# Kernel tuning notes

Measured on AMD Instinct MI355X. Metric: run time of the kernel, lower is better.

## Reference

```python
import jax, jax.numpy as jnp
import numpy as np

SIGMA = 1.0
MU = 1.0
STRIKE = 3.0
N_STEPS = 256
BATCH = 131072


def setup_inputs() -> dict:
    key = jax.random.key(0)
    ks = jax.random.split(key, 4)

    def lin(k, o, i):
        # equinox Linear-style uniform init in [-1/sqrt(i), 1/sqrt(i)]
        lim = 1.0 / np.sqrt(i)
        return jax.random.uniform(k, (o, i), jnp.float32, -lim, lim)

    return {
        "noise": jax.random.normal(ks[0], (N_STEPS, BATCH), jnp.float32),
        "ts": jnp.linspace(0.0, 1.0, N_STEPS + 1, dtype=jnp.float32),
        "w": jnp.float32(0.9),  # E[max(S1 - K, 0)] Monte-Carlo constant
        "W1": lin(ks[1], 32, 2), "b1": jnp.zeros((32,), jnp.float32),
        "W2": lin(ks[2], 32, 32), "b2": jnp.zeros((32,), jnp.float32),
        "W3": lin(ks[3], 1, 32), "b3": jnp.zeros((1,), jnp.float32),
    }


def reference(noise, ts, w, W1, b1, W2, b2, W3, b3):
    # Holding strategy MLP: in=[t, s] (2) -> 32 -> 32 -> 1, silu/silu/sigmoid
    def holding(t, s):  # s: [B] -> h: [B]
        x = jnp.stack([jnp.broadcast_to(t, s.shape), s], axis=-1)  # [B,2]
        a = jax.nn.silu(x @ W1.T + b1)
        a = jax.nn.silu(a @ W2.T + b2)
        return jax.nn.sigmoid(a @ W3.T + b3)[:, 0]

    def drift(t, y):  # y: [B,2] -> [B,2]
        s = y[:, 0]
        h = holding(t, s)
        return jnp.stack([MU * s, MU * s * h], axis=-1)

    def diffusion(t, y):  # scalar Brownian noise: diffusion vector [B,2]
        s = y[:, 0]
        h = holding(t, s)
        return jnp.stack([SIGMA * s, SIGMA * s * h], axis=-1)

    dts = jnp.diff(ts)                      # [N]
    dWs = noise * jnp.sqrt(dts)[:, None]    # [N,B] Brownian increments

    def step(y, xs):
        t, dt, dW = xs                      # dW: [B]
        f = drift(t, y)
        g = diffusion(t, y)
        # Milstein correction: directional derivative (Dg . g) via jvp
        _, dg = jax.jvp(lambda yy: diffusion(t, yy), (y,), (g,))
        y1 = (y + f * dt + g * dW[:, None]
              + 0.5 * dg * (dW * dW - dt)[:, None])  # Ito Milstein
        return y1, None

    B = noise.shape[1]
    y0 = jnp.broadcast_to(jnp.array([1.0, 0.0], jnp.float32), (B, 2))
    yT, _ = jax.lax.scan(step, y0, (ts[:-1], dts, dWs))

    s1 = yT[:, 0]
    hedging_pnl = yT[:, 1]
    z = jnp.maximum(0.0, s1 - STRIKE)
    return (z - hedging_pnl - w) ** 2  # [B] per-path loss
```

## Files before the change

kernel.cpp:

```cpp
#include <hip/hip_runtime.h>
#include <hip/hip_fp16.h>
#include <math.h>

#define BATCH 131072
#define NSTEPS 256
#define SEGLEN 64
#define NSEG 4
#define LGN 7
#define NPTS 128
#define ZSPAN 12.0f
#define ZLO 6.0f
#define ZSCALE (NPTS / ZSPAN)
#define DZ (ZSPAN / NPTS)
#define MU_C 0.72134752044448170367f
#define SD_C 1.4426950408889634f

using f32x2 = __attribute__((ext_vector_type(2))) float;

__device__ __forceinline__ float fast_exp(float x) {
    return __builtin_amdgcn_exp2f(x * 1.44269504088896340736f);
}
__device__ __forceinline__ float fast_rcp(float x) {
    return __builtin_amdgcn_rcpf(x);
}
__device__ __forceinline__ float sigmoidf_fast(float x) {
    return fast_rcp(1.0f + fast_exp(-x));
}

#define REP32(M) M(0) M(1) M(2) M(3) M(4) M(5) M(6) M(7) \
                 M(8) M(9) M(10) M(11) M(12) M(13) M(14) M(15) \
                 M(16) M(17) M(18) M(19) M(20) M(21) M(22) M(23) \
                 M(24) M(25) M(26) M(27) M(28) M(29) M(30) M(31)

#define REP8(M) M(0) M(1) M(2) M(3) M(4) M(5) M(6) M(7)

#define MLP_BODY(W1r, B1, W2r, B2, W3r, b3v, t, s, sd, H, HACC) \
    { \
        const float __t = (t), __s = (s), __sd = (sd); \
        f32x2 acc2 = {(b3v), 0.0f}; \
        REP32(MLP_L1) \
        REP32(MLP_ROW) \
        H = sigmoidf_fast(acc2.x); \
        HACC = acc2.y; \
    }

#define MLP_L1(j) f32x2 at##j; { \
    const float2 wv = W1r[j]; \
    const float z  = fmaf(wv.x, __t, fmaf(wv.y, __s, B1[j])); \
    const float zd = wv.y * __sd; \
    const float sg = sigmoidf_fast(z); \
    const float da = sg * (1.0f + z * (1.0f - sg)); \
    at##j = (f32x2){z * sg, da * zd}; }

#define MLP_ROW(j) { \
    const float4 q0 = W2r[(j) * 8 + 0]; \
    const float4 q1 = W2r[(j) * 8 + 1]; \
    const float4 q2 = W2r[(j) * 8 + 2]; \
    const float4 q3 = W2r[(j) * 8 + 3]; \
    const float4 q4 = W2r[(j) * 8 + 4]; \
    const float4 q5 = W2r[(j) * 8 + 5]; \
    const float4 q6 = W2r[(j) * 8 + 6]; \
    const float4 q7 = W2r[(j) * 8 + 7]; \
    f32x2 zza = {B2[j], 0.0f}; \
    f32x2 zzb = {0.0f, 0.0f}; \
    zza += (f32x2){q0.x, q0.x} * at0;  zzb += (f32x2){q0.y, q0.y} * at1; \
    zza += (f32x2){q0.z, q0.z} * at2;  zzb += (f32x2){q0.w, q0.w} * at3; \
    zza += (f32x2){q1.x, q1.x} * at4;  zzb += (f32x2){q1.y, q1.y} * at5; \
    zza += (f32x2){q1.z, q1.z} * at6;  zzb += (f32x2){q1.w, q1.w} * at7; \
    zza += (f32x2){q2.x, q2.x} * at8;  zzb += (f32x2){q2.y, q2.y} * at9; \
    zza += (f32x2){q2.z, q2.z} * at10; zzb += (f32x2){q2.w, q2.w} * at11; \
    zza += (f32x2){q3.x, q3.x} * at12; zzb += (f32x2){q3.y, q3.y} * at13; \
    zza += (f32x2){q3.z, q3.z} * at14; zzb += (f32x2){q3.w, q3.w} * at15; \
    zza += (f32x2){q4.x, q4.x} * at16; zzb += (f32x2){q4.y, q4.y} * at17; \
    zza += (f32x2){q4.z, q4.z} * at18; zzb += (f32x2){q4.w, q4.w} * at19; \
    zza += (f32x2){q5.x, q5.x} * at20; zzb += (f32x2){q5.y, q5.y} * at21; \
    zza += (f32x2){q5.z, q5.z} * at22; zzb += (f32x2){q5.w, q5.w} * at23; \
    zza += (f32x2){q6.x, q6.x} * at24; zzb += (f32x2){q6.y, q6.y} * at25; \
    zza += (f32x2){q6.z, q6.z} * at26; zzb += (f32x2){q6.w, q6.w} * at27; \
    zza += (f32x2){q7.x, q7.x} * at28; zzb += (f32x2){q7.y, q7.y} * at29; \
    zza += (f32x2){q7.z, q7.z} * at30; zzb += (f32x2){q7.w, q7.w} * at31; \
    const f32x2 zzt = zza + zzb; \
    const float zv  = zzt.x; \
    const float sg  = sigmoidf_fast(zv); \
    const float da  = sg * (1.0f + zv * (1.0f - sg)); \
    const float w3  = W3r[j]; \
    acc2 += (f32x2){w3, w3} * (f32x2){zv * sg, da * zzt.y}; \
}

__global__ __launch_bounds__(256) void table_eval_kernel(
    const float* __restrict__ ts,
    const float* __restrict__ W1, const float* __restrict__ b1,
    const float* __restrict__ W2, const float* __restrict__ b2,
    const float* __restrict__ W3, const float* __restrict__ b3,
    unsigned int* __restrict__ W)
{
    __shared__ __align__(16) float sW1[64];
    __shared__ float sb1[32];
    __shared__ __align__(16) float sW2[1024];
    __shared__ float sb2[32];
    __shared__ float sW3[32];
    __shared__ float sb3[1];

    const int tid = threadIdx.x;
    for (int i = tid; i < 1024; i += 256) sW2[i] = W2[i];
    if (tid < 64) sW1[tid] = W1[tid];
    if (tid < 32) { sb1[tid] = b1[tid]; sb2[tid] = b2[tid]; sW3[tid] = W3[tid]; }
    if (tid == 0) sb3[0] = b3[0];
    __syncthreads();

    const float2* W1r = (const float2*)sW1;
    const float*  B1  = sb1;
    const float4* W2r = (const float4*)sW2;
    const float*  B2  = sb2;
    const float*  W3r = sW3;
    const float   b3v = sb3[0];

    const int gid = blockIdx.x * 256 + tid;
    const int st = gid >> LGN;
    const int k  = gid & (NPTS - 1);

    const float t  = ts[st];
    const float mu = MU_C * t;
    const float sd = SD_C * __builtin_sqrtf(t) + 1e-4f;
    const float zz = fmaf((float)k, DZ, -ZLO);
    const float s  = __builtin_amdgcn_exp2f(fmaf(zz, sd, mu));

    float h, hacc;
    MLP_BODY(W1r, B1, W2r, B2, W3r, b3v, t, s, 1.0f, h, hacc)

    const float q = h * (1.0f - h) * hacc * s;
    __half2 p = __floats2half2_rn(h, q);
    const unsigned int pv = *(unsigned int*)&p;

    W[2 * gid] = pv;
    if (k > 0)         W[2 * gid - 1] = pv;
    if (k == NPTS - 1) W[2 * gid + 1] = pv;
}

__global__ __launch_bounds__(256) void prod_kernel(
    const float* __restrict__ noise,
    const float* __restrict__ ts,
    float* __restrict__ P)
{
    __shared__ float2 sdt[SEGLEN];
    const int g    = blockIdx.x >> 9;
    const int pblk = blockIdx.x & 511;
    const int tid  = threadIdx.x;
    const int sbase = g * SEGLEN;

    if (tid < SEGLEN) {
        const float t0 = ts[sbase + tid];
        const float dtv = ts[sbase + tid + 1] - t0;
        sdt[tid] = make_float2(dtv, __builtin_sqrtf(dtv));
    }
    __syncthreads();

    const int path = pblk * 256 + tid;
    const float* np_ = noise + (size_t)sbase * BATCH + path;

    float prod = 1.0f;
    #pragma unroll 8
    for (int k = 0; k < SEGLEN; ++k) {
        const float2 d = sdt[k];
        const float dW  = np_[(size_t)k * BATCH] * d.y;
        const float mil = 0.5f * fmaf(dW, dW, -d.x);
        const float A   = d.x + dW + mil;
        prod = fmaf(prod, A, prod);
    }
    P[(size_t)g * BATCH + path] = prod;
}

__global__ __launch_bounds__(256, 4) void seg_kernel(
    const float* __restrict__ noise,
    const float* __restrict__ ts,
    const uint2* __restrict__ T2,
    const float* __restrict__ P,
    float* __restrict__ pnlb,
    float* __restrict__ sT,
    float* __restrict__ out)
{
    __shared__ float4 sdt4[SEGLEN];
    __shared__ float  scr[SEGLEN];
    const int g    = blockIdx.x >> 9;
    const int pblk = blockIdx.x & 511;
    const int tid  = threadIdx.x;
    const int sbase = g * SEGLEN;

    if (tid < SEGLEN) {
        const float t0  = ts[sbase + tid];
        const float dtv = ts[sbase + tid + 1] - t0;
        const float sdv = SD_C * __builtin_sqrtf(t0) + 1e-4f;
        const float wp  = fast_rcp(sdv) * ZSCALE;
        const float cp  = ZLO * ZSCALE - MU_C * t0 * wp;
        sdt4[tid] = make_float4(dtv, __builtin_sqrtf(dtv), cp, wp);
        scr[tid]  = 0.69314718056f * fast_rcp(wp);
    }
    __syncthreads();

    const int path = pblk * 256 + tid;
    const float* np_ = noise + (size_t)sbase * BATCH + path;
    const float umax = (float)NPTS - 1.001f;

    float s = 1.0f;
    if (g > 0) s = P[path];
    if (g > 1) s *= P[BATCH + path];
    if (g > 2) s *= P[2 * BATCH + path];
    float pnl = 0.0f;

    #define NLD0(k) float n##k = np_[(size_t)(k) * BATCH];
    REP8(NLD0)
    #undef NLD0

    #pragma unroll 1
    for (int cc = 0; cc < SEGLEN / 8; ++cc) {
        const int coff = cc * 8;
        const int pfo  = min(coff + 8, SEGLEN - 8);
        const float* nb = np_ + (size_t)pfo * BATCH;

        #define NPF(k) const float m##k = nb[(size_t)(k) * BATCH];
        REP8(NPF)
        #undef NPF

        #define CHK(k) \
            const float4 dq##k = sdt4[coff + k]; \
            const float dW##k  = n##k * dq##k.y; \
            const float mil##k = 0.5f * fmaf(dW##k, dW##k, -dq##k.x); \
            const float Af##k  = dq##k.x + dW##k + mil##k; \
            const float sv##k  = s; \
            s = fmaf(s, Af##k, s); \
            const float Pv##k = sv##k * Af##k; \
            const float Qv##k = sv##k * mil##k; \
            const float x##k = __builtin_amdgcn_logf(sv##k); \
            const float u##k = \
                fminf(fmaxf(fmaf(x##k, dq##k.w, dq##k.z), 0.0f), umax); \
            const int   i0##k = (int)u##k; \
            const float f##k  = u##k - (float)i0##k; \
            const uint2 E##k = \
                T2[((size_t)(sbase + coff + k) << LGN) + i0##k];
        REP8(CHK)
        #undef CHK

        #define PNK(k) { \
            const float2 a0 = __half22float2(*(const __half2*)&E##k.x); \
            const float2 a1 = __half22float2(*(const __half2*)&E##k.y); \
            const float cr = scr[coff + k]; \
            const float uu = f##k; \
            const float m  = uu * uu; \
            const float n  = m * uu; \
            const float dh = a1.x - a0.x; \
            const float ba = fmaf(-2.0f, n, 3.0f * m); \
            const float bb = fmaf(-2.0f, m, uu) + n; \
            const float bc = n - m; \
            const float hh = fmaf(dh, ba, a0.x) + cr * fmaf(a0.y, bb, a1.y * bc); \
            const float qq = fmaf(uu, a1.y - a0.y, a0.y); \
            pnl = fmaf(hh, Pv##k, fmaf(qq, Qv##k, pnl)); }
        REP8(PNK)
        #undef PNK

        #define NRT(k) n##k = m##k;
        REP8(NRT)
        #undef NRT
    }

    if (g == 0) {
        out[path] = pnl;
    } else {
        pnlb[(size_t)(g - 1) * BATCH + path] = pnl;
    }
    if (g == 3) sT[path] = s;
}

__global__ __launch_bounds__(256) void fin_kernel(
    const float* __restrict__ pnlb, const float* __restrict__ sT,
    const float* __restrict__ wq, float* __restrict__ out)
{
    const int p = blockIdx.x * 256 + threadIdx.x;
    const float pnl = out[p] + pnlb[p] + pnlb[BATCH + p] + pnlb[2 * BATCH + p];
    const float z = fmaxf(0.0f, sT[p] - 3.0f);
    const float d = z - pnl - wq[0];
    out[p] = d * d;
}

__global__ __launch_bounds__(256, 3) void deep_hedging_direct(
    const float* __restrict__ noise, const float* __restrict__ ts,
    const float* __restrict__ w,
    const float* __restrict__ W1, const float* __restrict__ b1,
    const float* __restrict__ W2, const float* __restrict__ b2,
    const float* __restrict__ W3, const float* __restrict__ b3,
    float* __restrict__ out)
{
    __shared__ __align__(16) float sW1[64];
    __shared__ float sb1[32];
    __shared__ __align__(16) float sW2[1024];
    __shared__ float sb2[32];
    __shared__ float sW3[32];
    __shared__ float sb3w[2];
    __shared__ float sts[NSTEPS + 1];

    const int tid = threadIdx.x;
    for (int i = tid; i < 1024; i += 256) sW2[i] = W2[i];
    if (tid < 64) sW1[tid] = W1[tid];
    if (tid < 32) { sb1[tid] = b1[tid]; sb2[tid] = b2[tid]; sW3[tid] = W3[tid]; }
    if (tid == 0) { sb3w[0] = b3[0]; sb3w[1] = w[0]; }
    for (int i = tid; i < NSTEPS + 1; i += 256) sts[i] = ts[i];
    __syncthreads();

    const int gid = blockIdx.x * 256 + tid;
    const float* np_ = noise + gid;

    float s   = 1.0f;
    float pnl = 0.0f;
    const float b3v = sb3w[0];
    const float wv_ = sb3w[1];

    #pragma unroll 1
    for (int st = 0; st < NSTEPS; ++st) {
        int zr = 0;
        asm volatile("" : "+v"(zr));
        const float2* W1r = (const float2*)sW1 + zr;
        const float*  B1  = sb1 + zr;
        const float4* W2r = (const float4*)sW2 + zr;
        const float*  B2  = sb2 + zr;
        const float*  W3r = sW3 + zr;

        const float t  = sts[st];
        const float dt = sts[st + 1] - t;
        const float dW = np_[(size_t)st * BATCH] * __builtin_sqrtf(dt);
        const float sd = s;

        float h, hacc;
        MLP_BODY(W1r, B1, W2r, B2, W3r, b3v, t, s, sd, h, hacc)
        const float hd = h * (1.0f - h) * hacc;

        const float mil = 0.5f * (dW * dW - dt);
        const float g1  = s * h;
        const float dg1 = fmaf(sd, h, s * hd);
        const float snew = s + s * dt + s * dW + sd * mil;
        pnl = pnl + g1 * dt + g1 * dW + dg1 * mil;
        s = snew;
    }

    const float z = fmaxf(0.0f, s - 3.0f);
    const float d = z - pnl - wv_;
    out[gid] = d * d;
}

extern "C" void kernel_launch(void* const* d_in, const int* in_sizes, int n_in,
                              void* d_out, int out_size, void* d_ws, size_t ws_size,
                              hipStream_t stream) {
    const float* noise = (const float*)d_in[0];
    const float* ts    = (const float*)d_in[1];
    const float* w     = (const float*)d_in[2];
    const float* W1    = (const float*)d_in[3];
    const float* b1    = (const float*)d_in[4];
    const float* W2    = (const float*)d_in[5];
    const float* b2    = (const float*)d_in[6];
    const float* W3    = (const float*)d_in[7];
    const float* b3    = (const float*)d_in[8];
    float* out = (float*)d_out;

    const size_t tblB = (size_t)NSTEPS * NPTS * sizeof(uint2);
    const size_t pB   = (size_t)3 * BATCH * sizeof(float);
    const size_t need = tblB + 2 * pB + (size_t)BATCH * sizeof(float);

    if (ws_size >= need) {
        uint2* T2   = (uint2*)d_ws;
        float* P    = (float*)((char*)d_ws + tblB);
        float* pnlb = (float*)((char*)d_ws + tblB + pB);
        float* sT   = (float*)((char*)d_ws + tblB + 2 * pB);

        dim3 b(256);
        table_eval_kernel<<<dim3(NSTEPS * NPTS / 256), b, 0, stream>>>(
            ts, W1, b1, W2, b2, W3, b3, (unsigned int*)T2);
        prod_kernel<<<dim3(3 * BATCH / 256), b, 0, stream>>>(noise, ts, P);
        seg_kernel<<<dim3(4 * BATCH / 256), b, 0, stream>>>(
            noise, ts, T2, P, pnlb, sT, out);
        fin_kernel<<<dim3(BATCH / 256), b, 0, stream>>>(pnlb, sT, w, out);
    } else {
        dim3 grid(BATCH / 256), block(256);
        deep_hedging_direct<<<grid, block, 0, stream>>>(noise, ts, w, W1, b1,
                                                        W2, b2, W3, b3, out);
    }
}
```

Baseline: 72.64 us.

## Merge prefix-product pass into two-segment path kernel, drop prod_kernel

```diff
diff --git a/kernel.cpp b/kernel.cpp
--- a/kernel.cpp
+++ b/kernel.cpp
@@ -4,8 +4,7 @@
 
 #define BATCH 131072
 #define NSTEPS 256
-#define SEGLEN 64
-#define NSEG 4
+#define SEGLEN 128
 #define LGN 7
 #define NPTS 128
 #define ZSPAN 12.0f
@@ -137,52 +136,20 @@
     if (k == NPTS - 1) W[2 * gid + 1] = pv;
 }
 
-__global__ __launch_bounds__(256) void prod_kernel(
-    const float* __restrict__ noise,
-    const float* __restrict__ ts,
-    float* __restrict__ P)
-{
-    __shared__ float2 sdt[SEGLEN];
-    const int g    = blockIdx.x >> 9;
-    const int pblk = blockIdx.x & 511;
-    const int tid  = threadIdx.x;
-    const int sbase = g * SEGLEN;
-
-    if (tid < SEGLEN) {
-        const float t0 = ts[sbase + tid];
-        const float dtv = ts[sbase + tid + 1] - t0;
-        sdt[tid] = make_float2(dtv, __builtin_sqrtf(dtv));
-    }
-    __syncthreads();
-
-    const int path = pblk * 256 + tid;
-    const float* np_ = noise + (size_t)sbase * BATCH + path;
-
-    float prod = 1.0f;
-    #pragma unroll 8
-    for (int k = 0; k < SEGLEN; ++k) {
-        const float2 d = sdt[k];
-        const float dW  = np_[(size_t)k * BATCH] * d.y;
-        const float mil = 0.5f * fmaf(dW, dW, -d.x);
-        const float A   = d.x + dW + mil;
-        prod = fmaf(prod, A, prod);
-    }
-    P[(size_t)g * BATCH + path] = prod;
-}
-
-__global__ __launch_bounds__(256, 4) void seg_kernel(
+__global__ __launch_bounds__(256, 4) void path2_kernel(
     const float* __restrict__ noise,
     const float* __restrict__ ts,
     const uint2* __restrict__ T2,
-    const float* __restrict__ P,
+    float* __restrict__ out,
     float* __restrict__ pnlb,
-    float* __restrict__ sT,
-    float* __restrict__ out)
+    float* __restrict__ sT)
 {
     __shared__ float4 sdt4[SEGLEN];
     __shared__ float  scr[SEGLEN];
-    const int g    = blockIdx.x >> 9;
-    const int pblk = blockIdx.x & 511;
+    __shared__ float2 spre[SEGLEN];
+
+    const int g    = blockIdx.x & 1;
+    const int pblk = blockIdx.x >> 1;
     const int tid  = threadIdx.x;
     const int sbase = g * SEGLEN;
 
@@ -194,17 +161,38 @@
         const float cp  = ZLO * ZSCALE - MU_C * t0 * wp;
         sdt4[tid] = make_float4(dtv, __builtin_sqrtf(dtv), cp, wp);
         scr[tid]  = 0.69314718056f * fast_rcp(wp);
+    } else {
+        const int r = tid - SEGLEN;
+        const float t0  = ts[r];
+        const float dtv = ts[r + 1] - t0;
+        spre[r] = make_float2(dtv, __builtin_sqrtf(dtv));
     }
     __syncthreads();
 
     const int path = pblk * 256 + tid;
+    const float umax = (float)NPTS - 1.001f;
+
+    float s = 1.0f;
+    if (g) {
+        const float* npp = noise + path;
+        #pragma unroll 1
+        for (int c = 0; c < SEGLEN / 8; ++c) {
+            const int b0 = c * 8;
+            #define PLD(k) const float a##k = npp[(size_t)(b0 + k) * BATCH];
+            REP8(PLD)
+            #undef PLD
+            #define PCH(k) { \
+                const float2 d = spre[b0 + k]; \
+                const float dW  = a##k * d.y; \
+                const float mil = 0.5f * fmaf(dW, dW, -d.x); \
+                const float A   = d.x + dW + mil; \
+                s = fmaf(s, A, s); }
+            REP8(PCH)
+            #undef PCH
+        }
+    }
+
     const float* np_ = noise + (size_t)sbase * BATCH + path;
-    const float umax = (float)NPTS - 1.001f;
-
-    float s = 1.0f;
-    if (g > 0) s = P[path];
-    if (g > 1) s *= P[BATCH + path];
-    if (g > 2) s *= P[2 * BATCH + path];
     float pnl = 0.0f;
 
     #define NLD0(k) float n##k = np_[(size_t)(k) * BATCH];
@@ -265,9 +253,9 @@
     if (g == 0) {
         out[path] = pnl;
     } else {
-        pnlb[(size_t)(g - 1) * BATCH + path] = pnl;
-    }
-    if (g == 3) sT[path] = s;
+        pnlb[path] = pnl;
+        sT[path] = s;
+    }
 }
 
 __global__ __launch_bounds__(256) void fin_kernel(
@@ -275,7 +263,7 @@
     const float* __restrict__ wq, float* __restrict__ out)
 {
     const int p = blockIdx.x * 256 + threadIdx.x;
-    const float pnl = out[p] + pnlb[p] + pnlb[BATCH + p] + pnlb[2 * BATCH + p];
+    const float pnl = out[p] + pnlb[p];
     const float z = fmaxf(0.0f, sT[p] - 3.0f);
     const float d = z - pnl - wq[0];
     out[p] = d * d;
@@ -360,21 +348,19 @@
     float* out = (float*)d_out;
 
     const size_t tblB = (size_t)NSTEPS * NPTS * sizeof(uint2);
-    const size_t pB   = (size_t)3 * BATCH * sizeof(float);
-    const size_t need = tblB + 2 * pB + (size_t)BATCH * sizeof(float);
+    const size_t vecB = (size_t)BATCH * sizeof(float);
+    const size_t need = tblB + 2 * vecB;
 
     if (ws_size >= need) {
         uint2* T2   = (uint2*)d_ws;
-        float* P    = (float*)((char*)d_ws + tblB);
-        float* pnlb = (float*)((char*)d_ws + tblB + pB);
-        float* sT   = (float*)((char*)d_ws + tblB + 2 * pB);
+        float* pnlb = (float*)((char*)d_ws + tblB);
+        float* sT   = (float*)((char*)d_ws + tblB + vecB);
 
         dim3 b(256);
         table_eval_kernel<<<dim3(NSTEPS * NPTS / 256), b, 0, stream>>>(
             ts, W1, b1, W2, b2, W3, b3, (unsigned int*)T2);
-        prod_kernel<<<dim3(3 * BATCH / 256), b, 0, stream>>>(noise, ts, P);
-        seg_kernel<<<dim3(4 * BATCH / 256), b, 0, stream>>>(
-            noise, ts, T2, P, pnlb, sT, out);
+        path2_kernel<<<dim3(2 * BATCH / 256), b, 0, stream>>>(
+            noise, ts, T2, out, pnlb, sT);
         fin_kernel<<<dim3(BATCH / 256), b, 0, stream>>>(pnlb, sT, w, out);
     } else {
         dim3 grid(BATCH / 256), block(256);
```

Result: faster. 70.24 us (-3.3%).
